# Kernel optimization log

Measured on AMD Instinct MI355X. Metric: run time of the kernel, lower is better.

Reference implementation:

```python
import jax, jax.numpy as jnp
import numpy as np
from jax import lax

DIM = 512
E = 16
NC = 1000
ROUTER_TEMP = 1.0


def _conv(x, w, b):
    # NCHW conv, 3x3, SAME padding (matches nn.Conv2d(padding=1))
    y = lax.conv_general_dilated(x, w, (1, 1), 'SAME',
                                 dimension_numbers=('NCHW', 'OIHW', 'NCHW'))
    return y + b[None, :, None, None]


def _avgpool2(x):
    B, C, H, W = x.shape
    return x.reshape(B, C, H // 2, 2, W // 2, 2).mean(axis=(3, 5))


def setup_inputs() -> dict:
    key = jax.random.key(0)
    ks = jax.random.split(key, 12)
    B, C, H, W = 128, 3, 128, 128

    def init(k, shape, fan_in):
        return jax.random.normal(k, shape, jnp.float32) * (1.0 / np.sqrt(fan_in))

    return {
        'x': jax.random.normal(ks[0], (B, C, H, W), jnp.float32),
        'conv1_w': init(ks[1], (32, 3, 3, 3), 3 * 9),   'conv1_b': jnp.zeros((32,), jnp.float32),
        'conv2_w': init(ks[2], (32, 32, 3, 3), 32 * 9), 'conv2_b': jnp.zeros((32,), jnp.float32),
        'conv3_w': init(ks[3], (64, 32, 3, 3), 32 * 9), 'conv3_b': jnp.zeros((64,), jnp.float32),
        'conv4_w': init(ks[4], (64, 64, 3, 3), 64 * 9), 'conv4_b': jnp.zeros((64,), jnp.float32),
        'proj_w': init(ks[5], (64, DIM), 64),           'proj_b': jnp.zeros((DIM,), jnp.float32),
        'router_w': init(ks[6], (DIM, E), DIM),         'router_b': jnp.zeros((E,), jnp.float32),
        # stacked expert MLPs: Linear(dim,dim) -> ReLU -> Linear(dim,num_classes)
        'w1': init(ks[7], (E, DIM, DIM), DIM), 'b1': jnp.zeros((E, DIM), jnp.float32),
        'w2': init(ks[8], (E, DIM, NC), DIM),  'b2': jnp.zeros((E, NC), jnp.float32),
    }


def reference(x, conv1_w, conv1_b, conv2_w, conv2_b, conv3_w, conv3_b,
              conv4_w, conv4_b, proj_w, proj_b, router_w, router_b,
              w1, b1, w2, b2):
    # ---- Encoder ----
    h = jax.nn.relu(_conv(x, conv1_w, conv1_b))
    h = jax.nn.relu(_conv(h, conv2_w, conv2_b))
    h = _avgpool2(h)
    h = jax.nn.relu(_conv(h, conv3_w, conv3_b))
    h = _avgpool2(h)
    h = jax.nn.relu(_conv(h, conv4_w, conv4_b))
    h = h.mean(axis=(2, 3))                      # AdaptiveAvgPool2d(1) -> [B, 64]
    z = h @ proj_w + proj_b                      # [B, DIM]

    # ---- Router (top-1 gating) ----
    gate_logits = (z @ router_w + router_b) / ROUTER_TEMP   # [B, E]
    gate_probs = jax.nn.softmax(gate_logits, axis=-1)
    top1 = jnp.argmax(gate_probs, axis=-1)                  # [B] int
    B = z.shape[0]

    counts = lax.stop_gradient(
        jnp.zeros((E,), jnp.float32).at[top1].add(1.0) / B)
    importance = gate_probs.mean(axis=0)                    # [E]
    aux_loss = E * jnp.sum(counts * importance)

    # ---- Expert dispatch: gather per-token expert weights (top-1 hard routing) ----
    h1 = jax.nn.relu(jnp.einsum('bd,bdk->bk', z, w1[top1]) + b1[top1])   # [B, DIM]
    logits = jnp.einsum('bd,bdk->bk', h1, w2[top1]) + b2[top1]           # [B, NC]

    return logits, aux_loss, lax.stop_gradient(counts), lax.stop_gradient(importance)
```

## Files before the change

kernel.cpp:

```cpp
#include <hip/hip_runtime.h>
#include <math.h>

typedef unsigned short ushort_t;
typedef short short4x __attribute__((ext_vector_type(4)));
typedef short short8 __attribute__((ext_vector_type(8)));
typedef float f32x16 __attribute__((ext_vector_type(16)));

#define MFMA32(A,B,C) __builtin_amdgcn_mfma_f32_32x32x16_bf16(A,B,C,0,0,0)

__device__ __forceinline__ ushort_t f2bf(float f) {
    union { float f; unsigned u; } c; c.f = f;
    unsigned u = c.u;
    unsigned r = (u + 0x7FFFu + ((u >> 16) & 1u)) >> 16;
    return (ushort_t)r;
}

__device__ __forceinline__ unsigned pk2bf(float lo, float hi) {
    unsigned r;
    asm("v_cvt_pk_bf16_f32 %0, %1, %2" : "=v"(r) : "v"(lo), "v"(hi));
    return r;
}

template<int CTRL>
__device__ __forceinline__ float dppadd(float v) {
    int p = __builtin_amdgcn_mov_dpp(__builtin_bit_cast(int, v), CTRL, 0xF, 0xF, true);
    return v + __builtin_bit_cast(float, p);
}

__global__ __launch_bounds__(256) void k_wcvt(
    const float* __restrict__ c1w, const float* __restrict__ c1b_,
    const float* __restrict__ c2w, const float* __restrict__ c3w, const float* __restrict__ c4w,
    ushort_t* __restrict__ c1f, ushort_t* __restrict__ w2f,
    ushort_t* __restrict__ w3f, ushort_t* __restrict__ w4f,
    float* __restrict__ feat, float* __restrict__ tail)
{
    if (blockIdx.x == 33) {
        for (int i = threadIdx.x; i < 8192; i += 256) feat[i] = 0.f;
        if (threadIdx.x < 33) tail[threadIdx.x] = 0.f;
        return;
    }
    int r = blockIdx.x * 256 + threadIdx.x;
    int lane = r & 63, m = lane & 31, g = (lane >> 5) & 1;
    if (r < 1152) {
        int f = r >> 6, tau = f >> 1, h = f & 1, ky = tau / 3, kx = tau % 3;
        #pragma unroll
        for (int j = 0; j < 8; ++j) {
            int ic = h * 16 + g * 8 + j;
            w2f[r * 8 + j] = f2bf(0.25f * c2w[((m * 32 + ic) * 3 + ky) * 3 + kx]);
        }
    } else if (r < 3456) {
        int rr = r - 1152;
        int f = rr >> 6;
        int ot = f / 18, fl = f % 18, tau = fl >> 1, h = fl & 1, ky = tau / 3, kx = tau % 3;
        int oc = ot * 32 + m;
        #pragma unroll
        for (int j = 0; j < 8; ++j) {
            int ic = h * 16 + g * 8 + j;
            w3f[rr * 8 + j] = f2bf(0.25f * c3w[((oc * 32 + ic) * 3 + ky) * 3 + kx]);
        }
    } else if (r < 8064) {
        int rr = r - 3456;
        int f = rr >> 6;
        int ot = f / 36, fl = f % 36, tau = fl >> 2, h = fl & 3, ky = tau / 3, kx = tau % 3;
        int oc = ot * 32 + m;
        #pragma unroll
        for (int j = 0; j < 8; ++j) {
            int ic = h * 16 + g * 8 + j;
            w4f[rr * 8 + j] = f2bf(0.0009765625f * c4w[((oc * 64 + ic) * 3 + ky) * 3 + kx]);
        }
    } else if (r < 8256) {
        int rr = r - 8064;
        int f1 = rr >> 6;
        #pragma unroll
        for (int j = 0; j < 8; ++j) {
            int k = f1 * 16 + g * 8 + j;
            int p = k >> 2, c = k & 3;
            ushort_t v = 0;
            if (p < 9 && c < 3)
                v = f2bf(c1w[(m * 3 + c) * 9 + p]);
            else if (k == 3)
                v = f2bf(c1b_[m]);
            c1f[rr * 8 + j] = v;
        }
    }
}

__global__ __launch_bounds__(512, 4) void k_c12(
    const float* __restrict__ x,
    const ushort_t* __restrict__ c1f,
    const ushort_t* __restrict__ w2f, const float* __restrict__ c2b,
    ushort_t* __restrict__ a2)
{
    __shared__ __align__(16) ushort_t xs[1600];
    __shared__ __align__(16) ushort_t a1s[324 * 40];
    __shared__ float c2bs[32];
    const int t = threadIdx.x;
    const int bx = blockIdx.x, by = blockIdx.y, b = blockIdx.z;
    const int ox0 = bx * 16, oy0 = by * 16;

    if (t < 32) c2bs[t] = 0.25f * c2b[t];
    for (int i = t; i < 400; i += 512) {
        int yy = i / 20, xx = i % 20;
        int gy = oy0 - 2 + yy, gx = ox0 - 2 + xx;
        float v0 = 0.f, v1 = 0.f, v2 = 0.f;
        if (gy >= 0 && gy < 128 && gx >= 0 && gx < 128) {
            const float* px = x + ((size_t)(b * 3) * 128 + gy) * 128 + gx;
            v0 = px[0]; v1 = px[16384]; v2 = px[32768];
        }
        uint2 pk;
        pk.x = pk2bf(v0, v1);
        pk.y = pk2bf(v2, 1.0f);
        *(uint2*)&xs[i * 4] = pk;
    }

    const int wave = t >> 6, lane = t & 63;
    const int n = lane & 31, g = lane >> 5;

    short8 a1f0 = *(const short8*)(c1f + lane * 8);
    short8 a1f1 = *(const short8*)(c1f + (64 + lane) * 8);
    short8 a1f2 = *(const short8*)(c1f + (128 + lane) * 8);
    __syncthreads();

    for (int grp = wave; grp < 11; grp += 8) {
        int q = grp * 32 + n;
        bool qv = q < 324;
        int qc = qv ? q : 0;
        int cy = qc / 18, cx = qc % 18;
        int gy = oy0 - 1 + cy, gx = ox0 - 1 + cx;
        bool inimg = qv && gy >= 0 && gy < 128 && gx >= 0 && gx < 128;
        int base = (cy * 20 + cx) * 4;

        short4x q0 = *(const short4x*)&xs[base + (g ? 8 : 0)];
        short4x q1 = *(const short4x*)&xs[base + (g ? 80 : 4)];
        short4x q2 = *(const short4x*)&xs[base + (g ? 160 : 84)];
        short4x q3 = *(const short4x*)&xs[base + (g ? 164 : 88)];
        short4x q4 = *(const short4x*)&xs[base + 168];

        short8 b0 = __builtin_shufflevector(q0, q1, 0, 1, 2, 3, 4, 5, 6, 7);
        short8 b1 = __builtin_shufflevector(q2, q3, 0, 1, 2, 3, 4, 5, 6, 7);
        short8 b2 = __builtin_shufflevector(q4, q4, 0, 1, 2, 3, 0, 1, 2, 3);

        f32x16 acc;
        #pragma unroll
        for (int i = 0; i < 16; ++i) acc[i] = 0.f;
        acc = MFMA32(a1f0, b0, acc);
        acc = MFMA32(a1f1, b1, acc);
        acc = MFMA32(a1f2, b2, acc);

        if (qv) {
            ushort_t* dst = &a1s[q * 40 + 4 * g];
            #pragma unroll
            for (int qd = 0; qd < 4; ++qd) {
                float v0 = fmaxf(acc[qd * 4 + 0], 0.f);
                float v1 = fmaxf(acc[qd * 4 + 1], 0.f);
                float v2 = fmaxf(acc[qd * 4 + 2], 0.f);
                float v3 = fmaxf(acc[qd * 4 + 3], 0.f);
                uint2 pk;
                pk.x = inimg ? pk2bf(v0, v1) : 0u;
                pk.y = inimg ? pk2bf(v2, v3) : 0u;
                *(uint2*)&dst[8 * qd] = pk;
            }
        }
    }
    __syncthreads();

    const int x2 = (n >> 2) * 2 + (n & 1);
    const int y2 = wave * 2 + ((n >> 1) & 1);

    short8 af[18];
    #pragma unroll
    for (int f = 0; f < 18; ++f)
        af[f] = *(const short8*)(w2f + (f * 64 + lane) * 8);

    f32x16 acc;
    #pragma unroll
    for (int i = 0; i < 16; ++i) acc[i] = 0.f;

    const ushort_t* bbase = &a1s[(y2 * 18 + x2) * 40 + g * 8];
    #pragma unroll
    for (int tau = 0; tau < 9; ++tau) {
        const int off = ((tau / 3) * 18 + (tau % 3)) * 40;
        short8 b0 = *(const short8*)(bbase + off);
        short8 b1 = *(const short8*)(bbase + off + 16);
        acc = MFMA32(af[tau * 2 + 0], b0, acc);
        acc = MFMA32(af[tau * 2 + 1], b1, acc);
    }

    float pv[16];
    #pragma unroll
    for (int r = 0; r < 16; ++r) {
        float v = fmaxf(acc[r] + c2bs[(r & 3) + 8 * (r >> 2) + 4 * g], 0.f);
        v = dppadd<0xB1>(v);
        v = dppadd<0x4E>(v);
        pv[r] = v;
    }
    if ((n & 3) == 0) {
        const int poy = by * 8 + wave, pox = bx * 8 + (n >> 2);
        ushort_t* dst = &a2[(((size_t)b * 64 + poy) * 64 + pox) * 32 + 4 * g];
        #pragma unroll
        for (int qd = 0; qd < 4; ++qd) {
            uint2 pk;
            pk.x = pk2bf(pv[qd * 4 + 0], pv[qd * 4 + 1]);
            pk.y = pk2bf(pv[qd * 4 + 2], pv[qd * 4 + 3]);
            *(uint2*)&dst[8 * qd] = pk;
        }
    }
}

__global__ __launch_bounds__(512, 4) void k_c3(
    const ushort_t* __restrict__ a2, const ushort_t* __restrict__ w3f,
    const float* __restrict__ c3b, ushort_t* __restrict__ a3)
{
    __shared__ __align__(16) ushort_t s[324 * 40];
    __shared__ float bs[64];
    const int t = threadIdx.x;
    const int bx = blockIdx.x, by = blockIdx.y, b = blockIdx.z;
    const int x0 = bx * 16, y0 = by * 16;
    if (t < 64) bs[t] = 0.25f * c3b[t];
    for (int idx = t; idx < 1296; idx += 512) {
        int cell = idx >> 2, part = idx & 3;
        int cy = cell / 18, cx = cell % 18;
        int gy = y0 - 1 + cy, gx = x0 - 1 + cx;
        uint4 v = make_uint4(0, 0, 0, 0);
        if (gy >= 0 && gy < 64 && gx >= 0 && gx < 64)
            v = *(const uint4*)(a2 + (((size_t)b * 64 + gy) * 64 + gx) * 32 + part * 8);
        *(uint4*)(&s[cell * 40 + part * 8]) = v;
    }
    __syncthreads();

    const int wave = t >> 6, lane = t & 63;
    const int n = lane & 31, g = lane >> 5;
    const int x3 = (n >> 2) * 2 + (n & 1);
    const int y3 = wave * 2 + ((n >> 1) & 1);

    f32x16 acc0, acc1;
    #pragma unroll
    for (int i = 0; i < 16; ++i) { acc0[i] = 0.f; acc1[i] = 0.f; }

    const ushort_t* bbase = &s[(y3 * 18 + x3) * 40 + g * 8];
    #pragma unroll
    for (int tau = 0; tau < 9; ++tau) {
        const int off = ((tau / 3) * 18 + (tau % 3)) * 40;
        short8 b0 = *(const short8*)(bbase + off);
        short8 b1 = *(const short8*)(bbase + off + 16);
        short8 a00 = *(const short8*)(w3f + ((tau * 2 + 0) * 64 + lane) * 8);
        short8 a01 = *(const short8*)(w3f + ((tau * 2 + 1) * 64 + lane) * 8);
        short8 a10 = *(const short8*)(w3f + (((18 + tau * 2) + 0) * 64 + lane) * 8);
        short8 a11 = *(const short8*)(w3f + (((18 + tau * 2) + 1) * 64 + lane) * 8);
        acc0 = MFMA32(a00, b0, acc0);
        acc0 = MFMA32(a01, b1, acc0);
        acc1 = MFMA32(a10, b0, acc1);
        acc1 = MFMA32(a11, b1, acc1);
    }

    const int poy = by * 8 + wave, pox = bx * 8 + (n >> 2);
    ushort_t* dst = &a3[(((size_t)b * 32 + poy) * 32 + pox) * 64 + 4 * g];
    #pragma unroll
    for (int ot = 0; ot < 2; ++ot) {
        const f32x16& ac = ot ? acc1 : acc0;
        float pv[16];
        #pragma unroll
        for (int r = 0; r < 16; ++r) {
            float v = fmaxf(ac[r] + bs[ot * 32 + (r & 3) + 8 * (r >> 2) + 4 * g], 0.f);
            v = dppadd<0xB1>(v);
            v = dppadd<0x4E>(v);
            pv[r] = v;
        }
        if ((n & 3) == 0) {
            #pragma unroll
            for (int qd = 0; qd < 4; ++qd) {
                uint2 pk;
                pk.x = pk2bf(pv[qd * 4 + 0], pv[qd * 4 + 1]);
                pk.y = pk2bf(pv[qd * 4 + 2], pv[qd * 4 + 3]);
                *(uint2*)&dst[ot * 32 + 8 * qd] = pk;
            }
        }
    }
}

__global__ __launch_bounds__(512, 2) void k_c4(
    const ushort_t* __restrict__ a3, const ushort_t* __restrict__ w4f,
    const float* __restrict__ c4b, float* __restrict__ feat)
{
    __shared__ __align__(16) ushort_t s[324 * 72];
    __shared__ float bs[64];
    const int t = threadIdx.x;
    const int bx = blockIdx.x, by = blockIdx.y, b = blockIdx.z;
    const int x0 = bx * 16, y0 = by * 16;
    if (t < 64) bs[t] = 0.0009765625f * c4b[t];
    for (int idx = t; idx < 2592; idx += 512) {
        int cell = idx >> 3, part = idx & 7;
        int cy = cell / 18, cx = cell % 18;
        int gy = y0 - 1 + cy, gx = x0 - 1 + cx;
        uint4 v = make_uint4(0, 0, 0, 0);
        if (gy >= 0 && gy < 32 && gx >= 0 && gx < 32)
            v = *(const uint4*)(a3 + (((size_t)b * 32 + gy) * 32 + gx) * 64 + part * 8);
        *(uint4*)(&s[cell * 72 + part * 8]) = v;
    }
    __syncthreads();

    const int wave = t >> 6, lane = t & 63;
    const int n = lane & 31, g = lane >> 5;
    const int ry = n >> 4, rx = n & 15;
    const int y4 = wave * 2 + ry;

    f32x16 acc0, acc1;
    #pragma unroll
    for (int i = 0; i < 16; ++i) { acc0[i] = 0.f; acc1[i] = 0.f; }

    const ushort_t* bbase = &s[(y4 * 18 + rx) * 72 + g * 8];
    #pragma unroll
    for (int hp = 0; hp < 2; ++hp) {
        #pragma unroll
        for (int tau = 0; tau < 9; ++tau) {
            const int off = ((tau / 3) * 18 + (tau % 3)) * 72 + hp * 32;
            short8 b0 = *(const short8*)(bbase + off);
            short8 b1 = *(const short8*)(bbase + off + 16);
            short8 a00 = *(const short8*)(w4f + ((tau * 4 + hp * 2 + 0) * 64 + lane) * 8);
            short8 a01 = *(const short8*)(w4f + ((tau * 4 + hp * 2 + 1) * 64 + lane) * 8);
            short8 a10 = *(const short8*)(w4f + ((36 + tau * 4 + hp * 2 + 0) * 64 + lane) * 8);
            short8 a11 = *(const short8*)(w4f + ((36 + tau * 4 + hp * 2 + 1) * 64 + lane) * 8);
            acc0 = MFMA32(a00, b0, acc0);
            acc0 = MFMA32(a01, b1, acc0);
            acc1 = MFMA32(a10, b0, acc1);
            acc1 = MFMA32(a11, b1, acc1);
        }
    }

    #pragma unroll
    for (int ot = 0; ot < 2; ++ot) {
        const f32x16& ac = ot ? acc1 : acc0;
        #pragma unroll
        for (int r = 0; r < 16; ++r) {
            int oc = ot * 32 + (r & 3) + 8 * (r >> 2) + 4 * g;
            float v = fmaxf(ac[r] + bs[oc], 0.f);
            v = dppadd<0xB1>(v);
            v = dppadd<0x4E>(v);
            v += __shfl_xor(v, 4);
            v += __shfl_xor(v, 8);
            v += __shfl_xor(v, 16);
            if ((lane & 31) == 0)
                atomicAdd(&feat[b * 64 + oc], v);
        }
    }
}

__global__ __launch_bounds__(256) void k_router(
    const float* __restrict__ meanacc,
    const float* __restrict__ pw, const float* __restrict__ pb,
    const float* __restrict__ rw, const float* __restrict__ rb,
    ushort_t* __restrict__ zb, int* __restrict__ top1, float* __restrict__ tail)
{
    __shared__ float m[64];
    __shared__ float zs[512];
    __shared__ float part[256];
    __shared__ float gate[16];
    const int b = blockIdx.x, t = threadIdx.x;
    if (t < 64) m[t] = meanacc[b * 64 + t];
    __syncthreads();

    #pragma unroll
    for (int j = 0; j < 2; ++j) {
        int d = t + j * 256;
        float s = pb[d];
        for (int c = 0; c < 64; ++c) s += m[c] * pw[c * 512 + d];
        zs[d] = s;
        zb[b * 512 + d] = f2bf(s);
    }
    __syncthreads();
    {
        int e = t & 15, gg = t >> 4;
        float s = 0.f;
        for (int j = 0; j < 32; ++j) {
            int d = gg * 32 + j;
            s += zs[d] * rw[d * 16 + e];
        }
        part[t] = s;
    }
    __syncthreads();
    if (t < 16) {
        float s = rb[t];
        for (int gg = 0; gg < 16; ++gg) s += part[gg * 16 + t];
        gate[t] = s;
    }
    __syncthreads();
    if (t == 0) {
        float mx = gate[0];
        int am = 0;
        for (int e = 1; e < 16; ++e)
            if (gate[e] > mx) { mx = gate[e]; am = e; }
        float pr[16];
        float sum = 0.f;
        for (int e = 0; e < 16; ++e) { pr[e] = expf(gate[e] - mx); sum += pr[e]; }
        float inv = 1.f / sum;
        top1[b] = am;
        atomicAdd(&tail[1 + am], 1.0f / 128.0f);
        for (int e = 0; e < 16; ++e)
            atomicAdd(&tail[17 + e], pr[e] * inv * (1.0f / 128.0f));
    }
}

__global__ void k_sort(const int* __restrict__ top1, int* __restrict__ meta,
                       int* __restrict__ perm, float* __restrict__ tail)
{
    __shared__ int c[16], o[16], pos[128];
    const int t = threadIdx.x;
    if (t < 16) c[t] = 0;
    __syncthreads();
    int e = 0;
    if (t < 128) { e = top1[t]; pos[t] = atomicAdd(&c[e], 1); }
    __syncthreads();
    if (t == 0) {
        int s = 0;
        for (int i = 0; i < 16; ++i) { o[i] = s; s += c[i]; }
        int nt = 0;
        for (int i = 0; i < 16; ++i) {
            for (int r0 = 0; r0 < c[i]; r0 += 32) {
                meta[33 + nt] = i;
                meta[53 + nt] = o[i] + r0;
                int rem = c[i] - r0;
                meta[73 + nt] = rem < 32 ? rem : 32;
                ++nt;
            }
        }
        meta[32] = nt;
        for (int k = nt; k < 20; ++k) { meta[33 + k] = 0; meta[53 + k] = 0; meta[73 + k] = 0; }
        float s2 = 0.f;
        for (int i = 0; i < 16; ++i) s2 += tail[1 + i] * tail[17 + i];
        tail[0] = 16.0f * s2;
    }
    __syncthreads();
    if (t < 128) perm[o[e] + pos[t]] = t;
    if (t < 16) { meta[t] = c[t]; meta[16 + t] = o[t]; }
}

__global__ __launch_bounds__(64) void k_mlp1(
    const ushort_t* __restrict__ zb, const int* __restrict__ meta, const int* __restrict__ perm,
    const float* __restrict__ w1, const float* __restrict__ b1, ushort_t* __restrict__ h1b)
{
    const int ty = blockIdx.y;
    if (ty >= meta[32]) return;
    const int e = meta[33 + ty], ts = meta[53 + ty], rows = meta[73 + ty];
    const int n0 = blockIdx.x * 32;
    __shared__ __align__(16) ushort_t ws[32 * 520];
    __shared__ int tks[32];
    const int lane = threadIdx.x;
    const int mn = lane & 31, g = lane >> 5;

    if (lane < 32) tks[lane] = (lane < rows) ? perm[ts + lane] : -1;

    const float* Wg = w1 + ((size_t)e << 18) + n0;
    {
        const int cq = lane & 7, dg = lane >> 3;
        #pragma unroll 4
        for (int it = 0; it < 32; ++it) {
            int d = it * 16 + dg * 2;
            float4 va = *(const float4*)(Wg + (size_t)d * 512 + 4 * cq);
            float4 vb = *(const float4*)(Wg + (size_t)(d + 1) * 512 + 4 * cq);
            *(unsigned*)&ws[(4 * cq + 0) * 520 + d] = pk2bf(va.x, vb.x);
            *(unsigned*)&ws[(4 * cq + 1) * 520 + d] = pk2bf(va.y, vb.y);
            *(unsigned*)&ws[(4 * cq + 2) * 520 + d] = pk2bf(va.z, vb.z);
            *(unsigned*)&ws[(4 * cq + 3) * 520 + d] = pk2bf(va.w, vb.w);
        }
    }
    __syncthreads();

    const int tok_a = tks[mn] < 0 ? 0 : tks[mn];
    const ushort_t* za = zb + (size_t)tok_a * 512;

    f32x16 acc;
    #pragma unroll
    for (int i = 0; i < 16; ++i) acc[i] = 0.f;

    #pragma unroll 4
    for (int kt = 0; kt < 16; ++kt) {
        int k0 = kt * 32;
        short8 a0 = *(const short8*)(za + k0 + g * 8);
        short8 a1 = *(const short8*)(za + k0 + 16 + g * 8);
        short8 b0 = *(const short8*)(&ws[mn * 520 + k0 + g * 8]);
        short8 b1 = *(const short8*)(&ws[mn * 520 + k0 + 16 + g * 8]);
        acc = MFMA32(a0, b0, acc);
        acc = MFMA32(a1, b1, acc);
    }

    const float bias = b1[e * 512 + n0 + mn];
    #pragma unroll
    for (int r = 0; r < 16; ++r) {
        int mrow = (r & 3) + 8 * (r >> 2) + 4 * g;
        int tok = tks[mrow];
        if (tok >= 0) {
            float v = fmaxf(acc[r] + bias, 0.f);
            h1b[(size_t)tok * 512 + n0 + mn] = f2bf(v);
        }
    }
}

__global__ __launch_bounds__(64) void k_mlp2(
    const ushort_t* __restrict__ h1b, const int* __restrict__ meta, const int* __restrict__ perm,
    const float* __restrict__ w2, const float* __restrict__ b2, float* __restrict__ out)
{
    const int ty = blockIdx.y;
    if (ty >= meta[32]) return;
    const int e = meta[33 + ty], ts = meta[53 + ty], rows = meta[73 + ty];
    const int n0 = blockIdx.x * 32;
    __shared__ __align__(16) ushort_t ws[32 * 520];
    __shared__ int tks[32];
    const int lane = threadIdx.x;
    const int mn = lane & 31, g = lane >> 5;

    if (lane < 32) tks[lane] = (lane < rows) ? perm[ts + lane] : -1;

    const float* Wg = w2 + (size_t)e * 512000 + n0;
    {
        const int cq = lane & 7, dg = lane >> 3;
        const bool cut = (n0 == 992) && (cq >= 2);
        #pragma unroll 4
        for (int it = 0; it < 32; ++it) {
            int d = it * 16 + dg * 2;
            float4 va = make_float4(0.f, 0.f, 0.f, 0.f), vb = va;
            if (!cut) {
                va = *(const float4*)(Wg + (size_t)d * 1000 + 4 * cq);
                vb = *(const float4*)(Wg + (size_t)(d + 1) * 1000 + 4 * cq);
            }
            *(unsigned*)&ws[(4 * cq + 0) * 520 + d] = pk2bf(va.x, vb.x);
            *(unsigned*)&ws[(4 * cq + 1) * 520 + d] = pk2bf(va.y, vb.y);
            *(unsigned*)&ws[(4 * cq + 2) * 520 + d] = pk2bf(va.z, vb.z);
            *(unsigned*)&ws[(4 * cq + 3) * 520 + d] = pk2bf(va.w, vb.w);
        }
    }
    __syncthreads();

    const int tok_a = tks[mn] < 0 ? 0 : tks[mn];
    const ushort_t* ha = h1b + (size_t)tok_a * 512;

    f32x16 acc;
    #pragma unroll
    for (int i = 0; i < 16; ++i) acc[i] = 0.f;

    #pragma unroll 4
    for (int kt = 0; kt < 16; ++kt) {
        int k0 = kt * 32;
        short8 a0 = *(const short8*)(ha + k0 + g * 8);
        short8 a1 = *(const short8*)(ha + k0 + 16 + g * 8);
        short8 b0 = *(const short8*)(&ws[mn * 520 + k0 + g * 8]);
        short8 b1 = *(const short8*)(&ws[mn * 520 + k0 + 16 + g * 8]);
        acc = MFMA32(a0, b0, acc);
        acc = MFMA32(a1, b1, acc);
    }

    const int col = n0 + mn;
    if (col < 1000) {
        const float bias = b2[e * 1000 + col];
        #pragma unroll
        for (int r = 0; r < 16; ++r) {
            int mrow = (r & 3) + 8 * (r >> 2) + 4 * g;
            int tok = tks[mrow];
            if (tok >= 0)
                out[(size_t)tok * 1000 + col] = acc[r] + bias;
        }
    }
}

extern "C" void kernel_launch(void* const* d_in, const int* in_sizes, int n_in,
                              void* d_out, int out_size, void* d_ws, size_t ws_size,
                              hipStream_t stream)
{
    const float* x   = (const float*)d_in[0];
    const float* c1w = (const float*)d_in[1];
    const float* c1b = (const float*)d_in[2];
    const float* c2w = (const float*)d_in[3];
    const float* c2b = (const float*)d_in[4];
    const float* c3w = (const float*)d_in[5];
    const float* c3b = (const float*)d_in[6];
    const float* c4w = (const float*)d_in[7];
    const float* c4b = (const float*)d_in[8];
    const float* pw  = (const float*)d_in[9];
    const float* pb  = (const float*)d_in[10];
    const float* rw  = (const float*)d_in[11];
    const float* rb  = (const float*)d_in[12];
    const float* w1  = (const float*)d_in[13];
    const float* b1  = (const float*)d_in[14];
    const float* w2  = (const float*)d_in[15];
    const float* b2  = (const float*)d_in[16];

    float* out = (float*)d_out;
    float* tail = out + 128000;

    char* w = (char*)d_ws;
    ushort_t* a2   = (ushort_t*)(w);
    ushort_t* a3   = (ushort_t*)(w + 33554432);
    ushort_t* w2f  = (ushort_t*)(w + 50331648);
    ushort_t* w3f  = (ushort_t*)(w + 50350080);
    ushort_t* w4f  = (ushort_t*)(w + 50386944);
    ushort_t* c1f  = (ushort_t*)(w + 50460672);
    float*    feat = (float*)(w + 50464768);
    ushort_t* zb   = (ushort_t*)(w + 50497536);
    ushort_t* h1b  = (ushort_t*)(w + 50628608);
    int*      top1 = (int*)(w + 50759680);
    int*      meta = (int*)(w + 50760192);
    int*      perm = (int*)(w + 50760704);

    k_wcvt  <<<34, 256, 0, stream>>>(c1w, c1b, c2w, c3w, c4w, c1f, w2f, w3f, w4f, feat, tail);
    k_c12   <<<dim3(8, 8, 128), 512, 0, stream>>>(x, c1f, w2f, c2b, a2);
    k_c3    <<<dim3(4, 4, 128), 512, 0, stream>>>(a2, w3f, c3b, a3);
    k_c4    <<<dim3(2, 2, 128), 512, 0, stream>>>(a3, w4f, c4b, feat);
    k_router<<<128, 256, 0, stream>>>(feat, pw, pb, rw, rb, zb, top1, tail);
    k_sort  <<<1, 128, 0, stream>>>(top1, meta, perm, tail);
    k_mlp1  <<<dim3(16, 20), 64, 0, stream>>>(zb, meta, perm, w1, b1, h1b);
    k_mlp2  <<<dim3(32, 20), 64, 0, stream>>>(h1b, meta, perm, w2, b2, out);
}
```

Baseline: 192.9 us.

## Fold expert sort into MLP kernels and specialise interior conv tiles

Removes the separate single-block sort kernel launch. Each MLP block now recomputes the per-expert counts, tile map and permutation from top1 in shared memory, and the aux loss is computed in one mlp1 block. Separately, the conv1/conv2 kernel takes a branch-free path for interior tiles, skipping bounds checks on input loads and the in-image mask. The cost is redundant per-block prelude work: 16 lanes each scan 128 tokens twice, adding serial latency to every MLP block.

```diff
diff --git a/kernel.cpp b/kernel.cpp
--- a/kernel.cpp
+++ b/kernel.cpp
@@ -97,20 +97,32 @@
     const int t = threadIdx.x;
     const int bx = blockIdx.x, by = blockIdx.y, b = blockIdx.z;
     const int ox0 = bx * 16, oy0 = by * 16;
+    const bool interior = ((unsigned)(bx - 1) < 6u) && ((unsigned)(by - 1) < 6u);
 
     if (t < 32) c2bs[t] = 0.25f * c2b[t];
-    for (int i = t; i < 400; i += 512) {
-        int yy = i / 20, xx = i % 20;
-        int gy = oy0 - 2 + yy, gx = ox0 - 2 + xx;
-        float v0 = 0.f, v1 = 0.f, v2 = 0.f;
-        if (gy >= 0 && gy < 128 && gx >= 0 && gx < 128) {
-            const float* px = x + ((size_t)(b * 3) * 128 + gy) * 128 + gx;
-            v0 = px[0]; v1 = px[16384]; v2 = px[32768];
-        }
-        uint2 pk;
-        pk.x = pk2bf(v0, v1);
-        pk.y = pk2bf(v2, 1.0f);
-        *(uint2*)&xs[i * 4] = pk;
+    if (interior) {
+        for (int i = t; i < 400; i += 512) {
+            int yy = i / 20, xx = i % 20;
+            const float* px = x + ((size_t)(b * 3) * 128 + (oy0 - 2 + yy)) * 128 + (ox0 - 2 + xx);
+            uint2 pk;
+            pk.x = pk2bf(px[0], px[16384]);
+            pk.y = pk2bf(px[32768], 1.0f);
+            *(uint2*)&xs[i * 4] = pk;
+        }
+    } else {
+        for (int i = t; i < 400; i += 512) {
+            int yy = i / 20, xx = i % 20;
+            int gy = oy0 - 2 + yy, gx = ox0 - 2 + xx;
+            float v0 = 0.f, v1 = 0.f, v2 = 0.f;
+            if (gy >= 0 && gy < 128 && gx >= 0 && gx < 128) {
+                const float* px = x + ((size_t)(b * 3) * 128 + gy) * 128 + gx;
+                v0 = px[0]; v1 = px[16384]; v2 = px[32768];
+            }
+            uint2 pk;
+            pk.x = pk2bf(v0, v1);
+            pk.y = pk2bf(v2, 1.0f);
+            *(uint2*)&xs[i * 4] = pk;
+        }
     }
 
     const int wave = t >> 6, lane = t & 63;
@@ -121,13 +133,16 @@
     short8 a1f2 = *(const short8*)(c1f + (128 + lane) * 8);
     __syncthreads();
 
-    for (int grp = wave; grp < 11; grp += 8) {
+    auto conv1_group = [&](int grp) {
         int q = grp * 32 + n;
         bool qv = q < 324;
         int qc = qv ? q : 0;
         int cy = qc / 18, cx = qc % 18;
-        int gy = oy0 - 1 + cy, gx = ox0 - 1 + cx;
-        bool inimg = qv && gy >= 0 && gy < 128 && gx >= 0 && gx < 128;
+        bool inimg = qv;
+        if (!interior) {
+            int gy = oy0 - 1 + cy, gx = ox0 - 1 + cx;
+            inimg = qv && gy >= 0 && gy < 128 && gx >= 0 && gx < 128;
+        }
         int base = (cy * 20 + cx) * 4;
 
         short4x q0 = *(const short4x*)&xs[base + (g ? 8 : 0)];
@@ -161,7 +176,9 @@
                 *(uint2*)&dst[8 * qd] = pk;
             }
         }
-    }
+    };
+    conv1_group(wave);
+    if (wave < 3) conv1_group(wave + 8);
     __syncthreads();
 
     const int x2 = (n >> 2) * 2 + (n & 1);
@@ -400,51 +417,69 @@
     }
 }
 
-__global__ void k_sort(const int* __restrict__ top1, int* __restrict__ meta,
-                       int* __restrict__ perm, float* __restrict__ tail)
-{
-    __shared__ int c[16], o[16], pos[128];
-    const int t = threadIdx.x;
-    if (t < 16) c[t] = 0;
-    __syncthreads();
-    int e = 0;
-    if (t < 128) { e = top1[t]; pos[t] = atomicAdd(&c[e], 1); }
-    __syncthreads();
-    if (t == 0) {
-        int s = 0;
-        for (int i = 0; i < 16; ++i) { o[i] = s; s += c[i]; }
-        int nt = 0;
+struct TileMap {
+    int e, ts, rows, nt;
+};
+__device__ __forceinline__ TileMap tile_prelude(
+    const int* __restrict__ top1, int ty, int lane,
+    int* cnt, int* o, int* tkE, int* tkS, int* tkR, int* perm, int* ntS)
+{
+    if (lane < 16) {
+        int cc = 0;
+        for (int tok = 0; tok < 128; ++tok) cc += (top1[tok] == lane) ? 1 : 0;
+        cnt[lane] = cc;
+    }
+    __syncthreads();
+    if (lane == 0) {
+        int s = 0, nt = 0;
         for (int i = 0; i < 16; ++i) {
-            for (int r0 = 0; r0 < c[i]; r0 += 32) {
-                meta[33 + nt] = i;
-                meta[53 + nt] = o[i] + r0;
-                int rem = c[i] - r0;
-                meta[73 + nt] = rem < 32 ? rem : 32;
+            o[i] = s;
+            int ci = cnt[i];
+            for (int r0 = 0; r0 < ci; r0 += 32) {
+                tkE[nt] = i; tkS[nt] = s + r0;
+                int rem = ci - r0; tkR[nt] = rem < 32 ? rem : 32;
                 ++nt;
             }
-        }
-        meta[32] = nt;
-        for (int k = nt; k < 20; ++k) { meta[33 + k] = 0; meta[53 + k] = 0; meta[73 + k] = 0; }
-        float s2 = 0.f;
-        for (int i = 0; i < 16; ++i) s2 += tail[1 + i] * tail[17 + i];
-        tail[0] = 16.0f * s2;
-    }
-    __syncthreads();
-    if (t < 128) perm[o[e] + pos[t]] = t;
-    if (t < 16) { meta[t] = c[t]; meta[16 + t] = o[t]; }
+            s += ci;
+        }
+        *ntS = nt;
+    }
+    __syncthreads();
+    if (lane < 16) {
+        int cur = o[lane];
+        for (int tok = 0; tok < 128; ++tok)
+            if (top1[tok] == lane) perm[cur++] = tok;
+    }
+    __syncthreads();
+    TileMap tm;
+    tm.nt = *ntS;
+    if (ty < tm.nt) { tm.e = tkE[ty]; tm.ts = tkS[ty]; tm.rows = tkR[ty]; }
+    else { tm.e = 0; tm.ts = 0; tm.rows = 0; }
+    return tm;
 }
 
 __global__ __launch_bounds__(64) void k_mlp1(
-    const ushort_t* __restrict__ zb, const int* __restrict__ meta, const int* __restrict__ perm,
-    const float* __restrict__ w1, const float* __restrict__ b1, ushort_t* __restrict__ h1b)
-{
-    const int ty = blockIdx.y;
-    if (ty >= meta[32]) return;
-    const int e = meta[33 + ty], ts = meta[53 + ty], rows = meta[73 + ty];
-    const int n0 = blockIdx.x * 32;
+    const ushort_t* __restrict__ zb, const int* __restrict__ top1,
+    const float* __restrict__ w1, const float* __restrict__ b1,
+    ushort_t* __restrict__ h1b, float* __restrict__ tail)
+{
+    __shared__ int cnt[16], o[16], tkE[20], tkS[20], tkR[20], perm[128], ntS;
     __shared__ __align__(16) ushort_t ws[32 * 520];
     __shared__ int tks[32];
     const int lane = threadIdx.x;
+    const int ty = blockIdx.y;
+
+    TileMap tm = tile_prelude(top1, ty, lane, cnt, o, tkE, tkS, tkR, perm, &ntS);
+
+    if (blockIdx.x == 0 && ty == 0 && lane == 0) {
+        float s2 = 0.f;
+        for (int i = 0; i < 16; ++i)
+            s2 += ((float)cnt[i] * (1.0f / 128.0f)) * tail[17 + i];
+        tail[0] = 16.0f * s2;
+    }
+    if (ty >= tm.nt) return;
+    const int e = tm.e, ts = tm.ts, rows = tm.rows;
+    const int n0 = blockIdx.x * 32;
     const int mn = lane & 31, g = lane >> 5;
 
     if (lane < 32) tks[lane] = (lane < rows) ? perm[ts + lane] : -1;
@@ -496,16 +531,19 @@
 }
 
 __global__ __launch_bounds__(64) void k_mlp2(
-    const ushort_t* __restrict__ h1b, const int* __restrict__ meta, const int* __restrict__ perm,
+    const ushort_t* __restrict__ h1b, const int* __restrict__ top1,
     const float* __restrict__ w2, const float* __restrict__ b2, float* __restrict__ out)
 {
-    const int ty = blockIdx.y;
-    if (ty >= meta[32]) return;
-    const int e = meta[33 + ty], ts = meta[53 + ty], rows = meta[73 + ty];
-    const int n0 = blockIdx.x * 32;
+    __shared__ int cnt[16], o[16], tkE[20], tkS[20], tkR[20], perm[128], ntS;
     __shared__ __align__(16) ushort_t ws[32 * 520];
     __shared__ int tks[32];
     const int lane = threadIdx.x;
+    const int ty = blockIdx.y;
+
+    TileMap tm = tile_prelude(top1, ty, lane, cnt, o, tkE, tkS, tkR, perm, &ntS);
+    if (ty >= tm.nt) return;
+    const int e = tm.e, ts = tm.ts, rows = tm.rows;
+    const int n0 = blockIdx.x * 32;
     const int mn = lane & 31, g = lane >> 5;
 
     if (lane < 32) tks[lane] = (lane < rows) ? perm[ts + lane] : -1;
@@ -597,15 +635,12 @@
     ushort_t* zb   = (ushort_t*)(w + 50497536);
     ushort_t* h1b  = (ushort_t*)(w + 50628608);
     int*      top1 = (int*)(w + 50759680);
-    int*      meta = (int*)(w + 50760192);
-    int*      perm = (int*)(w + 50760704);
 
     k_wcvt  <<<34, 256, 0, stream>>>(c1w, c1b, c2w, c3w, c4w, c1f, w2f, w3f, w4f, feat, tail);
     k_c12   <<<dim3(8, 8, 128), 512, 0, stream>>>(x, c1f, w2f, c2b, a2);
     k_c3    <<<dim3(4, 4, 128), 512, 0, stream>>>(a2, w3f, c3b, a3);
     k_c4    <<<dim3(2, 2, 128), 512, 0, stream>>>(a3, w4f, c4b, feat);
     k_router<<<128, 256, 0, stream>>>(feat, pw, pb, rw, rb, zb, top1, tail);
-    k_sort  <<<1, 128, 0, stream>>>(top1, meta, perm, tail);
-    k_mlp1  <<<dim3(16, 20), 64, 0, stream>>>(zb, meta, perm, w1, b1, h1b);
-    k_mlp2  <<<dim3(32, 20), 64, 0, stream>>>(h1b, meta, perm, w2, b2, out);
-}
+    k_mlp1  <<<dim3(16, 20), 64, 0, stream>>>(zb, top1, w1, b1, h1b, tail);
+    k_mlp2  <<<dim3(32, 20), 64, 0, stream>>>(h1b, top1, w2, b2, out);
+}
```

After: 209.6 us. +8.6%, slower.
